# Kernel optimization log

Hardware: AMD Instinct MI355X
Metric: run time of the kernel (lower is better)

Reference implementation:

```python
import jax, jax.numpy as jnp
import numpy as np

B, S, A, M, H, OUT = 256, 256, 256, 256, 8, 256
KD = A // H   # key_dim per head = 32
VD = M // H   # value_dim per head = 32


def setup_inputs() -> dict:
    key = jax.random.key(0)
    ks = jax.random.split(key, 11)
    return {
        "q_data": jax.random.normal(ks[0], (B, S, A), dtype=jnp.float32),
        "m_data": jax.random.normal(ks[1], (B, S, M), dtype=jnp.float32),
        "bias": jax.random.normal(ks[2], (B, 1, 1, S), dtype=jnp.float32),
        "nonbatched_bias": jax.random.normal(ks[3], (H, S, S), dtype=jnp.float32),
        "query_w": jax.random.normal(ks[4], (A, H, KD), dtype=jnp.float32) * 0.05,
        "key_w": jax.random.normal(ks[5], (M, H, KD), dtype=jnp.float32) * 0.05,
        "value_w": jax.random.normal(ks[6], (M, H, VD), dtype=jnp.float32) * 0.05,
        "gating_w": jax.random.normal(ks[7], (A, H, VD), dtype=jnp.float32) * 0.05,
        "gating_b": jax.random.normal(ks[8], (H, VD), dtype=jnp.float32) * 0.05,
        "output_w": jax.random.normal(ks[9], (H, VD, OUT), dtype=jnp.float32) * 0.05,
        "output_b": jax.random.normal(ks[10], (OUT,), dtype=jnp.float32) * 0.05,
    }


def reference(q_data, m_data, bias, nonbatched_bias,
              query_w, key_w, value_w, gating_w, gating_b, output_w, output_b):
    key_dim = query_w.shape[-1]
    # projections
    q = jnp.einsum('bqa,ahc->bqhc', q_data, query_w) * key_dim ** (-0.5)
    k = jnp.einsum('bka,ahc->bkhc', m_data, key_w)
    v = jnp.einsum('bka,ahc->bkhc', m_data, value_w)
    # logits [b,h,q,k] with batched + shared bias
    logits = jnp.einsum('bqhc,bkhc->bhqk', q, k) + bias + nonbatched_bias[None]
    weights = jax.nn.softmax(logits, axis=-1)
    weighted_avg = jnp.einsum('bhqk,bkhc->bqhc', weights, v)
    # sigmoid gating
    gate_values = jax.nn.sigmoid(jnp.einsum('bqc,chv->bqhv', q_data, gating_w) + gating_b)
    weighted_avg = weighted_avg * gate_values
    # output projection
    output = jnp.einsum('bqhc,hco->bqo', weighted_avg, output_w) + output_b
    return output
```

## Files before the change

### kernel.cpp

```cpp
#include <hip/hip_runtime.h>

typedef unsigned short u16;
typedef __attribute__((ext_vector_type(8))) short short8;
typedef __attribute__((ext_vector_type(4))) float f32x4;
typedef __attribute__((ext_vector_type(4))) unsigned int u32x4;
typedef __attribute__((ext_vector_type(4))) unsigned short u16x4;

#define LOG2E 1.4426950408889634f

__device__ __forceinline__ float bf2f(u16 u) {
    union { float f; unsigned int i; } c; c.i = ((unsigned int)u) << 16; return c.f;
}
__device__ __forceinline__ u16 f2bf(float f) {
    unsigned int x = __float_as_uint(f);
    x += 0x7fff + ((x >> 16) & 1);
    return (u16)(x >> 16);
}
__device__ __forceinline__ unsigned int cvtpk(float lo, float hi) {
    unsigned int d;
    asm("v_cvt_pk_bf16_f32 %0, %1, %2" : "=v"(d) : "v"(lo), "v"(hi));
    return d;
}

union Cvt32 { u32x4 v[4]; u16 u[32]; };

__device__ __forceinline__ void ld32f_bf(const float* __restrict__ p, Cvt32& t) {
    union { unsigned int i[8]; u32x4 v[2]; } a;
#pragma unroll
    for (int j = 0; j < 4; j++) {
        f32x4 x = *(const f32x4*)(p + j * 4);
        a.i[j * 2]     = cvtpk(x[0], x[1]);
        a.i[j * 2 + 1] = cvtpk(x[2], x[3]);
    }
    t.v[0] = a.v[0]; t.v[1] = a.v[1];
#pragma unroll
    for (int j = 0; j < 4; j++) {
        f32x4 x = *(const f32x4*)(p + 16 + j * 4);
        a.i[j * 2]     = cvtpk(x[0], x[1]);
        a.i[j * 2 + 1] = cvtpk(x[2], x[3]);
    }
    t.v[2] = a.v[0]; t.v[3] = a.v[1];
}


__global__ __launch_bounds__(256) void prep_a(
    const float* __restrict__ nb,
    const float* __restrict__ qw, const float* __restrict__ kw,
    const float* __restrict__ vw, const float* __restrict__ gw,
    const float* __restrict__ ow,
    u16* __restrict__ wt, u16* __restrict__ WoT, u16* __restrict__ nbT)
{
    __shared__ float tile[64][65];
    int blk = blockIdx.x, tid = threadIdx.x;
    if (blk < 1024) {
        int i = blk * 256 + tid;
        int half = i >> 17;
        int rem = i & 131071;
        int h = rem >> 14, e = rem & 16383;
        int n = e >> 8, k = e & 255;
        int src_idx = k * 256 + h * 32 + (n & 31);
        float v;
        if (half == 0) v = (n < 32) ? kw[src_idx] : vw[src_idx];
        else           v = (n < 32) ? qw[src_idx] : gw[src_idx];
        wt[i] = f2bf(v);
    } else if (blk < 1280) {
        int e = (blk - 1024) * 256 + tid;
        int o = e & 255, hc = e >> 8;
        WoT[o * 256 + hc] = f2bf(ow[hc * 256 + o]);
    } else {
        int idx = blk - 1280;
        int q0 = (idx & 3) * 64, k0 = ((idx >> 2) & 3) * 64, h = idx >> 4;
        int rr = tid >> 4;
        int cc = (tid & 15) << 2;
        const float* src = nb + ((size_t)(h * 256 + q0)) * 256 + k0;
#pragma unroll
        for (int p = 0; p < 4; p++) {
            int q = rr + p * 16;
            f32x4 x = *(const f32x4*)(src + (size_t)q * 256 + cc);
            tile[q][cc] = x[0]; tile[q][cc + 1] = x[1];
            tile[q][cc + 2] = x[2]; tile[q][cc + 3] = x[3];
        }
        __syncthreads();
        u16* dst = nbT + ((size_t)(h * 256 + k0)) * 256 + q0;
#pragma unroll
        for (int p = 0; p < 4; p++) {
            int k = rr + p * 16;
            u16x4 o;
#pragma unroll
            for (int u = 0; u < 4; u++) o[u] = f2bf(tile[cc + u][k] * LOG2E);
            *(u16x4*)(dst + (size_t)k * 256 + cc) = o;
        }
    }
}

__global__ __launch_bounds__(256) void fusedA(
    const float* __restrict__ q_data, const float* __restrict__ m_data,
    const float* __restrict__ bias2, const u16* __restrict__ nbT,
    const u16* __restrict__ wt, const float* __restrict__ gb,
    u16* __restrict__ WA)
{
    __shared__ u16 smem[31488];
    u16* Ksh = smem;
    u16* Vt  = smem + 10240;
    u16* Xs  = smem + 18688;
    u16* Wsh = smem + 28928;

    int bid = blockIdx.x;
    int b = bid >> 3, h = bid & 7;
    int tid = threadIdx.x, lane = tid & 63, w = tid >> 6;
    int l15 = lane & 15;
    int kl = (lane >> 4) << 3;
    int rq = (lane >> 4) << 2;
    const f32x4 fz = {0.f, 0.f, 0.f, 0.f};

    float bload[16];
#pragma unroll
    for (int t = 0; t < 16; t++)
        bload[t] = bias2[(b << 8) + t * 16 + l15] * LOG2E;
    float gbc0 = gb[h * 32 + l15];
    float gbc1 = gb[h * 32 + 16 + l15];

    const float* Xg = m_data + ((size_t)b << 16);
    const u16* Wg = wt + (h << 14);
    f32x4 acc[4][4];
#pragma unroll
    for (int i = 0; i < 4; i++)
#pragma unroll
        for (int j = 0; j < 4; j++) acc[i][j] = fz;

    for (int kb = 0; kb < 8; ++kb) {
        Cvt32 am;
        ld32f_bf(Xg + (size_t)tid * 256 + kb * 32, am);
        u32x4 b0, b1;
        int nrow = tid >> 1, nc = (tid & 1) << 4;
        if (tid < 128) {
            const u16* q = Wg + nrow * 256 + kb * 32 + nc;
            b0 = *(const u32x4*)q; b1 = *(const u32x4*)(q + 8);
        }
        if (kb) __syncthreads();
        *(u32x4*)&Xs[tid * 40]      = am.v[0];
        *(u32x4*)&Xs[tid * 40 + 8]  = am.v[1];
        *(u32x4*)&Xs[tid * 40 + 16] = am.v[2];
        *(u32x4*)&Xs[tid * 40 + 24] = am.v[3];
        if (tid < 128) {
            *(u32x4*)&Wsh[nrow * 40 + nc] = b0;
            *(u32x4*)&Wsh[nrow * 40 + nc + 8] = b1;
        }
        __syncthreads();
        short8 af[4], bf[4];
#pragma unroll
        for (int i = 0; i < 4; i++) af[i] = *(const short8*)&Xs[(64 * w + i * 16 + l15) * 40 + kl];
#pragma unroll
        for (int i = 0; i < 4; i++) bf[i] = *(const short8*)&Wsh[(i * 16 + l15) * 40 + kl];
#pragma unroll
        for (int mi = 0; mi < 4; mi++)
#pragma unroll
            for (int ni = 0; ni < 4; ni++)
                acc[mi][ni] = __builtin_amdgcn_mfma_f32_16x16x32_bf16(af[mi], bf[ni], acc[mi][ni], 0, 0, 0);
    }
#pragma unroll
    for (int mi = 0; mi < 4; mi++)
#pragma unroll
        for (int ni = 0; ni < 4; ni++)
#pragma unroll
            for (int r = 0; r < 4; r++) {
                int s = 64 * w + mi * 16 + rq + r;
                int col = ni * 16 + l15;
                u16 v = f2bf(acc[mi][ni][r]);
                if (ni < 2) Ksh[s * 40 + col] = v;
                else        Vt[(col - 32) * 264 + s] = v;
            }
    __syncthreads();

    const float* Xg2 = q_data + ((size_t)b << 16);
    const u16* Wg2 = wt + 131072 + (h << 14);
    f32x4 acc2[4][4];
#pragma unroll
    for (int i = 0; i < 4; i++)
#pragma unroll
        for (int j = 0; j < 4; j++) acc2[i][j] = fz;

    for (int kb = 0; kb < 8; ++kb) {
        Cvt32 am;
        ld32f_bf(Xg2 + (size_t)tid * 256 + kb * 32, am);
        u32x4 b0, b1;
        int nrow = tid >> 1, nc = (tid & 1) << 4;
        if (tid < 128) {
            const u16* q = Wg2 + nrow * 256 + kb * 32 + nc;
            b0 = *(const u32x4*)q; b1 = *(const u32x4*)(q + 8);
        }
        __syncthreads();
        *(u32x4*)&Xs[tid * 40]      = am.v[0];
        *(u32x4*)&Xs[tid * 40 + 8]  = am.v[1];
        *(u32x4*)&Xs[tid * 40 + 16] = am.v[2];
        *(u32x4*)&Xs[tid * 40 + 24] = am.v[3];
        if (tid < 128) {
            *(u32x4*)&Wsh[nrow * 40 + nc] = b0;
            *(u32x4*)&Wsh[nrow * 40 + nc + 8] = b1;
        }
        __syncthreads();
        short8 af[4], bf[4];
#pragma unroll
        for (int i = 0; i < 4; i++) af[i] = *(const short8*)&Xs[(64 * w + i * 16 + l15) * 40 + kl];
#pragma unroll
        for (int i = 0; i < 4; i++) bf[i] = *(const short8*)&Wsh[(i * 16 + l15) * 40 + kl];
#pragma unroll
        for (int mi = 0; mi < 4; mi++)
#pragma unroll
            for (int ni = 0; ni < 4; ni++)
                acc2[mi][ni] = __builtin_amdgcn_mfma_f32_16x16x32_bf16(af[mi], bf[ni], acc2[mi][ni], 0, 0, 0);
    }
    __syncthreads();

    u16* myQ = smem + 18688 + w * 1792;
    u16* myP = myQ + 640;
    const u16* nbh = nbT + ((size_t)h << 16);
    const float qs = 0.17677669529663687f * LOG2E;
    int orow = lane >> 2, ocol = (lane & 3) << 3;

#pragma unroll
    for (int mt = 0; mt < 4; ++mt) {
        int q0 = 64 * w + mt * 16 + rq;
#pragma unroll
        for (int ni = 0; ni < 2; ++ni)
#pragma unroll
            for (int r = 0; r < 4; r++)
                myQ[(rq + r) * 40 + ni * 16 + l15] = f2bf(acc2[mt][ni][r] * qs);
        short8 qf = *(const short8*)&myQ[l15 * 40 + kl];

        const u16* nbp = nbh + q0;
        float srow[4] = {0.f, 0.f, 0.f, 0.f};
        f32x4 oacc[2] = {fz, fz};
#pragma unroll
        for (int qt = 0; qt < 4; ++qt) {
            f32x4 sc[4];
#pragma unroll
            for (int t = 0; t < 4; t++) {
                int tt = qt * 4 + t;
                short8 kfr = *(const short8*)&Ksh[(tt * 16 + l15) * 40 + kl];
                f32x4 cb = {bload[tt], bload[tt], bload[tt], bload[tt]};
                sc[t] = __builtin_amdgcn_mfma_f32_16x16x32_bf16(qf, kfr, cb, 0, 0, 0);
            }
#pragma unroll
            for (int t = 0; t < 4; t++) {
                int tt = qt * 4 + t;
                u16x4 nbv = *(const u16x4*)(nbp + ((tt * 16 + l15) << 8));
#pragma unroll
                for (int r = 0; r < 4; r++) {
                    float p = __builtin_amdgcn_exp2f(sc[t][r] + bf2f(nbv[r]));
                    srow[r] += p;
                    myP[(rq + r) * 72 + t * 16 + l15] = f2bf(p);
                }
            }
#pragma unroll
            for (int ks = 0; ks < 2; ++ks) {
                short8 pf = *(const short8*)&myP[l15 * 72 + ks * 32 + kl];
#pragma unroll
                for (int ni = 0; ni < 2; ++ni) {
                    short8 vf = *(const short8*)&Vt[(ni * 16 + l15) * 264 + qt * 64 + ks * 32 + kl];
                    oacc[ni] = __builtin_amdgcn_mfma_f32_16x16x32_bf16(pf, vf, oacc[ni], 0, 0, 0);
                }
            }
        }
#pragma unroll
        for (int r = 0; r < 4; r++) {
            float s = srow[r];
            s += __shfl_xor(s, 1);
            s += __shfl_xor(s, 2);
            s += __shfl_xor(s, 4);
            s += __shfl_xor(s, 8);
            srow[r] = __builtin_amdgcn_rcpf(s);
        }

#pragma unroll
        for (int ni = 0; ni < 2; ++ni) {
            float gbv = ni ? gbc1 : gbc0;
#pragma unroll
            for (int r = 0; r < 4; r++) {
                float gate = __builtin_amdgcn_rcpf(
                    1.f + __builtin_amdgcn_exp2f(-(acc2[mt][ni + 2][r] + gbv) * LOG2E));
                myP[(rq + r) * 40 + ni * 16 + l15] = f2bf(oacc[ni][r] * srow[r] * gate);
            }
        }
        u32x4 ov = *(const u32x4*)&myP[orow * 40 + ocol];
        *(u32x4*)(WA + ((size_t)((b << 8) + 64 * w + mt * 16 + orow) << 8) + h * 32 + ocol) = ov;
    }
}

__global__ __launch_bounds__(256) void gemmout_a(
    const u16* __restrict__ WA, const u16* __restrict__ WoT,
    float* __restrict__ dst, const float* __restrict__ ob)
{
    __shared__ u16 As[128 * 40];
    __shared__ u16 Bs[128 * 40];
    int tid = threadIdx.x;
    int lane = tid & 63, w = tid >> 6;
    int wm = w >> 1, wn = w & 1;
    int row0 = blockIdx.x * 128;
    int n0 = blockIdx.y * 128;
    int lr = tid >> 1;
    int lc = (tid & 1) << 4;

    const f32x4 fz = {0.f, 0.f, 0.f, 0.f};
    f32x4 acc[4][4];
#pragma unroll
    for (int i = 0; i < 4; i++)
#pragma unroll
        for (int j = 0; j < 4; j++) acc[i][j] = fz;

    int kl = (lane >> 4) << 3;
    int l15 = lane & 15;
    int rm = wm * 64 + l15;
    int rn = wn * 64 + l15;

    for (int kb = 0; kb < 8; ++kb) {
        int k0 = kb << 5;
        const u16* pa = WA + ((size_t)(row0 + lr) << 8) + k0 + lc;
        u32x4 a0 = *(const u32x4*)pa;
        u32x4 a1 = *(const u32x4*)(pa + 8);
        const u16* pb = WoT + ((size_t)(n0 + lr) << 8) + k0 + lc;
        u32x4 b0 = *(const u32x4*)pb;
        u32x4 b1 = *(const u32x4*)(pb + 8);
        if (kb) __syncthreads();
        *(u32x4*)&As[lr * 40 + lc] = a0;
        *(u32x4*)&As[lr * 40 + lc + 8] = a1;
        *(u32x4*)&Bs[lr * 40 + lc] = b0;
        *(u32x4*)&Bs[lr * 40 + lc + 8] = b1;
        __syncthreads();
        short8 af[4], bf[4];
#pragma unroll
        for (int i = 0; i < 4; i++) af[i] = *(const short8*)&As[(rm + i * 16) * 40 + kl];
#pragma unroll
        for (int i = 0; i < 4; i++) bf[i] = *(const short8*)&Bs[(rn + i * 16) * 40 + kl];
#pragma unroll
        for (int mi = 0; mi < 4; mi++)
#pragma unroll
            for (int ni = 0; ni < 4; ni++)
                acc[mi][ni] = __builtin_amdgcn_mfma_f32_16x16x32_bf16(af[mi], bf[ni], acc[mi][ni], 0, 0, 0);
    }

#pragma unroll
    for (int mi = 0; mi < 4; mi++)
#pragma unroll
        for (int ni = 0; ni < 4; ni++)
#pragma unroll
            for (int r = 0; r < 4; r++) {
                int row = row0 + wm * 64 + mi * 16 + ((lane >> 4) << 2) + r;
                int col = n0 + wn * 64 + ni * 16 + l15;
                dst[((size_t)row << 8) + col] = acc[mi][ni][r] + ob[col];
            }
}


__global__ __launch_bounds__(256) void transpose_k(
    const float* __restrict__ query_w, const float* __restrict__ key_w,
    const float* __restrict__ value_w, const float* __restrict__ gating_w,
    u16* __restrict__ wt)
{
    int i = blockIdx.x * 256 + threadIdx.x;
    int half = i >> 17;
    int rem = i & 131071;
    int h = rem >> 14, e = rem & 16383;
    int n = e >> 8, k = e & 255;
    int src_idx = k * 256 + h * 32 + (n & 31);
    float v;
    if (half == 0) v = (n < 32) ? key_w[src_idx]   : value_w[src_idx];
    else           v = (n < 32) ? query_w[src_idx] : gating_w[src_idx];
    wt[i] = f2bf(v);
}

__global__ __launch_bounds__(256) void fused_attn_k(
    const float* __restrict__ q_data, const float* __restrict__ m_data,
    const float* __restrict__ bias2, const float* __restrict__ nb,
    const u16* __restrict__ wt, const float* __restrict__ gb,
    u16* __restrict__ WAo)
{
    __shared__ u16 smem[31488];
    u16* Ksh = smem;
    u16* Vt  = smem + 10240;
    u16* Xs  = smem + 18688;
    u16* Wsh = smem + 28928;

    int bid = blockIdx.x;
    int b = bid >> 3, h = bid & 7;
    int tid = threadIdx.x, lane = tid & 63, w = tid >> 6;
    int l15 = lane & 15;
    int kl = (lane >> 4) << 3;
    int rq = (lane >> 4) << 2;
    const f32x4 fz = {0.f, 0.f, 0.f, 0.f};

    float bload[16];
#pragma unroll
    for (int t = 0; t < 16; t++) bload[t] = bias2[(b << 8) + t * 16 + l15];
    float gbc0 = gb[h * 32 + l15];
    float gbc1 = gb[h * 32 + 16 + l15];

    const float* Xg = m_data + ((size_t)b << 16);
    const u16* Wg = wt + (h << 14);
    f32x4 acc[4][4];
#pragma unroll
    for (int i = 0; i < 4; i++)
#pragma unroll
        for (int j = 0; j < 4; j++) acc[i][j] = fz;

    for (int kb = 0; kb < 8; ++kb) {
        Cvt32 am;
        ld32f_bf(Xg + (size_t)tid * 256 + kb * 32, am);
        u32x4 b0, b1;
        int nrow = tid >> 1, nc = (tid & 1) << 4;
        if (tid < 128) {
            const u16* q = Wg + nrow * 256 + kb * 32 + nc;
            b0 = *(const u32x4*)q; b1 = *(const u32x4*)(q + 8);
        }
        if (kb) __syncthreads();
        *(u32x4*)&Xs[tid * 40]      = am.v[0];
        *(u32x4*)&Xs[tid * 40 + 8]  = am.v[1];
        *(u32x4*)&Xs[tid * 40 + 16] = am.v[2];
        *(u32x4*)&Xs[tid * 40 + 24] = am.v[3];
        if (tid < 128) {
            *(u32x4*)&Wsh[nrow * 40 + nc] = b0;
            *(u32x4*)&Wsh[nrow * 40 + nc + 8] = b1;
        }
        __syncthreads();
        short8 af[4], bf[4];
#pragma unroll
        for (int i = 0; i < 4; i++) af[i] = *(const short8*)&Xs[(64 * w + i * 16 + l15) * 40 + kl];
#pragma unroll
        for (int i = 0; i < 4; i++) bf[i] = *(const short8*)&Wsh[(i * 16 + l15) * 40 + kl];
#pragma unroll
        for (int mi = 0; mi < 4; mi++)
#pragma unroll
            for (int ni = 0; ni < 4; ni++)
                acc[mi][ni] = __builtin_amdgcn_mfma_f32_16x16x32_bf16(af[mi], bf[ni], acc[mi][ni], 0, 0, 0);
    }
#pragma unroll
    for (int mi = 0; mi < 4; mi++)
#pragma unroll
        for (int ni = 0; ni < 4; ni++)
#pragma unroll
            for (int r = 0; r < 4; r++) {
                int s = 64 * w + mi * 16 + rq + r;
                int col = ni * 16 + l15;
                u16 v = f2bf(acc[mi][ni][r]);
                if (ni < 2) Ksh[s * 40 + col] = v;
                else        Vt[(col - 32) * 264 + s] = v;
            }
    __syncthreads();

    const float* Xg2 = q_data + ((size_t)b << 16);
    const u16* Wg2 = wt + 131072 + (h << 14);
    f32x4 acc2[4][4];
#pragma unroll
    for (int i = 0; i < 4; i++)
#pragma unroll
        for (int j = 0; j < 4; j++) acc2[i][j] = fz;

    for (int kb = 0; kb < 8; ++kb) {
        Cvt32 am;
        ld32f_bf(Xg2 + (size_t)tid * 256 + kb * 32, am);
        u32x4 b0, b1;
        int nrow = tid >> 1, nc = (tid & 1) << 4;
        if (tid < 128) {
            const u16* q = Wg2 + nrow * 256 + kb * 32 + nc;
            b0 = *(const u32x4*)q; b1 = *(const u32x4*)(q + 8);
        }
        __syncthreads();
        *(u32x4*)&Xs[tid * 40]      = am.v[0];
        *(u32x4*)&Xs[tid * 40 + 8]  = am.v[1];
        *(u32x4*)&Xs[tid * 40 + 16] = am.v[2];
        *(u32x4*)&Xs[tid * 40 + 24] = am.v[3];
        if (tid < 128) {
            *(u32x4*)&Wsh[nrow * 40 + nc] = b0;
            *(u32x4*)&Wsh[nrow * 40 + nc + 8] = b1;
        }
        __syncthreads();
        short8 af[4], bf[4];
#pragma unroll
        for (int i = 0; i < 4; i++) af[i] = *(const short8*)&Xs[(64 * w + i * 16 + l15) * 40 + kl];
#pragma unroll
        for (int i = 0; i < 4; i++) bf[i] = *(const short8*)&Wsh[(i * 16 + l15) * 40 + kl];
#pragma unroll
        for (int mi = 0; mi < 4; mi++)
#pragma unroll
            for (int ni = 0; ni < 4; ni++)
                acc2[mi][ni] = __builtin_amdgcn_mfma_f32_16x16x32_bf16(af[mi], bf[ni], acc2[mi][ni], 0, 0, 0);
    }
    __syncthreads();

    u16* myQ = smem + 18688 + w * 2816;
    u16* myP = myQ + 640;
    const float* nbp = nb + ((size_t)h << 16);
    const float qscale = 0.17677669529663687f;

#pragma unroll
    for (int mt = 0; mt < 4; ++mt) {
#pragma unroll
        for (int ni = 0; ni < 2; ++ni)
#pragma unroll
            for (int r = 0; r < 4; r++)
                myQ[(rq + r) * 40 + ni * 16 + l15] = f2bf(acc2[mt][ni][r] * qscale);

        short8 qf = *(const short8*)&myQ[l15 * 40 + kl];
        f32x4 sc[16];
#pragma unroll
        for (int t = 0; t < 16; t++) {
            short8 kfr = *(const short8*)&Ksh[(t * 16 + l15) * 40 + kl];
            sc[t] = __builtin_amdgcn_mfma_f32_16x16x32_bf16(qf, kfr, fz, 0, 0, 0);
        }

        int q0 = 64 * w + mt * 16 + rq;
        float mrow[4] = {-3e30f, -3e30f, -3e30f, -3e30f};
#pragma unroll
        for (int t = 0; t < 16; t++) {
            int kidx = t * 16 + l15;
#pragma unroll
            for (int r = 0; r < 4; r++) {
                float v = sc[t][r] + bload[t] + nbp[(size_t)(q0 + r) * 256 + kidx];
                sc[t][r] = v;
                mrow[r] = fmaxf(mrow[r], v);
            }
        }
#pragma unroll
        for (int r = 0; r < 4; r++) {
            float m = mrow[r];
            m = fmaxf(m, __shfl_xor(m, 1));
            m = fmaxf(m, __shfl_xor(m, 2));
            m = fmaxf(m, __shfl_xor(m, 4));
            m = fmaxf(m, __shfl_xor(m, 8));
            mrow[r] = m;
        }
        float srow[4] = {0.f, 0.f, 0.f, 0.f};
#pragma unroll
        for (int t = 0; t < 16; t++)
#pragma unroll
            for (int r = 0; r < 4; r++) {
                float p = __expf(sc[t][r] - mrow[r]);
                sc[t][r] = p;
                srow[r] += p;
            }
#pragma unroll
        for (int r = 0; r < 4; r++) {
            float s = srow[r];
            s += __shfl_xor(s, 1);
            s += __shfl_xor(s, 2);
            s += __shfl_xor(s, 4);
            s += __shfl_xor(s, 8);
            srow[r] = 1.f / s;
        }

        f32x4 oacc[2] = {fz, fz};
#pragma unroll
        for (int half = 0; half < 2; ++half) {
#pragma unroll
            for (int t = 0; t < 8; t++)
#pragma unroll
                for (int r = 0; r < 4; r++)
                    myP[(rq + r) * 136 + t * 16 + l15] =
                        f2bf(sc[half * 8 + t][r] * srow[r]);
#pragma unroll
            for (int ks = 0; ks < 4; ++ks) {
                short8 pf = *(const short8*)&myP[l15 * 136 + ks * 32 + kl];
#pragma unroll
                for (int ni = 0; ni < 2; ++ni) {
                    short8 vf = *(const short8*)&Vt[(ni * 16 + l15) * 264 + half * 128 + ks * 32 + kl];
                    oacc[ni] = __builtin_amdgcn_mfma_f32_16x16x32_bf16(pf, vf, oacc[ni], 0, 0, 0);
                }
            }
        }

#pragma unroll
        for (int ni = 0; ni < 2; ++ni) {
            float gbv = ni ? gbc1 : gbc0;
#pragma unroll
            for (int r = 0; r < 4; r++) {
                float gate = 1.f / (1.f + __expf(-(acc2[mt][ni + 2][r] + gbv)));
                size_t idx = (((size_t)b << 8) + q0 + r) * 256 + h * 32 + ni * 16 + l15;
                WAo[idx] = f2bf(oacc[ni][r] * gate);
            }
        }
    }
}

__global__ __launch_bounds__(256) void gemm_out_k(
    const u16* __restrict__ X, const float* __restrict__ Wo,
    float* __restrict__ dst, const float* __restrict__ cbias)
{
    __shared__ u16 As[128 * 40];
    __shared__ u16 Bs[128 * 40];
    int tid = threadIdx.x;
    int lane = tid & 63, w = tid >> 6;
    int wm = w >> 1, wn = w & 1;
    int row0 = blockIdx.x * 128;
    int n0 = blockIdx.y * 128;
    int lr = tid >> 1;
    int lc = (tid & 1) << 4;

    const f32x4 fz = {0.f, 0.f, 0.f, 0.f};
    f32x4 acc[4][4];
#pragma unroll
    for (int i = 0; i < 4; i++)
#pragma unroll
        for (int j = 0; j < 4; j++) acc[i][j] = fz;

    int kl = (lane >> 4) << 3;
    int l15 = lane & 15;
    int rm = wm * 64 + l15;
    int rn = wn * 64 + l15;

    for (int kb = 0; kb < 8; ++kb) {
        int k0 = kb << 5;
        const u16* pa = X + ((size_t)(row0 + lr) << 8) + k0 + lc;
        u32x4 a0 = *(const u32x4*)pa;
        u32x4 a1 = *(const u32x4*)(pa + 8);
        int bk = tid >> 3, bn = (tid & 7) << 4;
        const float* pb = Wo + (size_t)(k0 + bk) * 256 + n0 + bn;
        u16 bu[16];
#pragma unroll
        for (int j = 0; j < 16; j += 4) {
            f32x4 x = *(const f32x4*)(pb + j);
            bu[j] = f2bf(x[0]); bu[j + 1] = f2bf(x[1]);
            bu[j + 2] = f2bf(x[2]); bu[j + 3] = f2bf(x[3]);
        }
        if (kb) __syncthreads();
        *(u32x4*)&As[lr * 40 + lc] = a0;
        *(u32x4*)&As[lr * 40 + lc + 8] = a1;
#pragma unroll
        for (int j = 0; j < 16; j++) Bs[(bn + j) * 40 + bk] = bu[j];
        __syncthreads();
        short8 af[4], bf[4];
#pragma unroll
        for (int i = 0; i < 4; i++) af[i] = *(const short8*)&As[(rm + i * 16) * 40 + kl];
#pragma unroll
        for (int i = 0; i < 4; i++) bf[i] = *(const short8*)&Bs[(rn + i * 16) * 40 + kl];
#pragma unroll
        for (int mi = 0; mi < 4; mi++)
#pragma unroll
            for (int ni = 0; ni < 4; ni++)
                acc[mi][ni] = __builtin_amdgcn_mfma_f32_16x16x32_bf16(af[mi], bf[ni], acc[mi][ni], 0, 0, 0);
    }

#pragma unroll
    for (int mi = 0; mi < 4; mi++)
#pragma unroll
        for (int ni = 0; ni < 4; ni++)
#pragma unroll
            for (int r = 0; r < 4; r++) {
                int row = row0 + wm * 64 + mi * 16 + ((lane >> 4) << 2) + r;
                int col = n0 + wn * 64 + ni * 16 + l15;
                dst[((size_t)row << 8) + col] = acc[mi][ni][r] + cbias[col];
            }
}

extern "C" void kernel_launch(void* const* d_in, const int* in_sizes, int n_in,
                              void* d_out, int out_size, void* d_ws, size_t ws_size,
                              hipStream_t stream)
{
    const float* q_data   = (const float*)d_in[0];
    const float* m_data   = (const float*)d_in[1];
    const float* bias     = (const float*)d_in[2];
    const float* nb       = (const float*)d_in[3];
    const float* query_w  = (const float*)d_in[4];
    const float* key_w    = (const float*)d_in[5];
    const float* value_w  = (const float*)d_in[6];
    const float* gating_w = (const float*)d_in[7];
    const float* gating_b = (const float*)d_in[8];
    const float* output_w = (const float*)d_in[9];
    const float* output_b = (const float*)d_in[10];

    const size_t NEED_A = 4ull * 33554432 + 524288 + 131072 + 1048576;

    if (ws_size >= NEED_A) {
        u16* ws   = (u16*)d_ws;
        u16* WA   = ws;
        u16* wt   = WA + 16777216;
        u16* WoT  = wt + 262144;
        u16* nbT  = WoT + 65536;

        prep_a<<<1408, 256, 0, stream>>>(nb, query_w, key_w, value_w, gating_w,
                                         output_w, wt, WoT, nbT);
        fusedA<<<2048, 256, 0, stream>>>(q_data, m_data, bias, nbT, wt, gating_b, WA);
        gemmout_a<<<dim3(512, 2), 256, 0, stream>>>(WA, WoT, (float*)d_out, output_b);
    } else {
        u16* WAb = (u16*)d_ws;
        u16* wt  = (u16*)d_out;
        transpose_k<<<1024, 256, 0, stream>>>(query_w, key_w, value_w, gating_w, wt);
        fused_attn_k<<<2048, 256, 0, stream>>>(q_data, m_data, bias, nb, wt, gating_b, WAb);
        gemm_out_k<<<dim3(512, 2), 256, 0, stream>>>(WAb, output_w, (float*)d_out, output_b);
    }
}
```

Measured before the change: 413.8 us.

## Reorder fusedA projections to alias K into staging LDS and raise occupancy

```diff
diff --git a/kernel.cpp b/kernel.cpp
--- a/kernel.cpp
+++ b/kernel.cpp
@@ -93,17 +93,17 @@
     }
 }
 
-__global__ __launch_bounds__(256) void fusedA(
+__global__ __launch_bounds__(256, 3) void fusedA(
     const float* __restrict__ q_data, const float* __restrict__ m_data,
     const float* __restrict__ bias2, const u16* __restrict__ nbT,
     const u16* __restrict__ wt, const float* __restrict__ gb,
     u16* __restrict__ WA)
 {
-    __shared__ u16 smem[31488];
-    u16* Ksh = smem;
-    u16* Vt  = smem + 10240;
-    u16* Xs  = smem + 18688;
-    u16* Wsh = smem + 28928;
+    __shared__ u16 smem[25856];
+    u16* Vt  = smem;
+    u16* Xs  = smem + 8448;
+    u16* Ksh = Xs;
+    u16* Wsh = smem + 18688;
 
     int bid = blockIdx.x;
     int b = bid >> 3, h = bid & 7;
@@ -120,6 +120,63 @@
     float gbc0 = gb[h * 32 + l15];
     float gbc1 = gb[h * 32 + 16 + l15];
 
+    int srow = tid >> 1;
+    int sc16 = (tid & 1) << 4;
+    int nrow = tid >> 1, nc = (tid & 1) << 4;
+
+    const float* Xg2 = q_data + ((size_t)b << 16);
+    const u16* Wg2 = wt + 131072 + (h << 14);
+    f32x4 acc2[4][4];
+#pragma unroll
+    for (int i = 0; i < 4; i++)
+#pragma unroll
+        for (int j = 0; j < 4; j++) acc2[i][j] = fz;
+
+    for (int kb = 0; kb < 8; ++kb) {
+        u32x4 c0[2], c1[2];
+#pragma unroll
+        for (int p = 0; p < 2; ++p) {
+            const float* ps = Xg2 + (size_t)(p * 128 + srow) * 256 + kb * 32 + sc16;
+            f32x4 x0 = *(const f32x4*)ps;
+            f32x4 x1 = *(const f32x4*)(ps + 4);
+            f32x4 x2 = *(const f32x4*)(ps + 8);
+            f32x4 x3 = *(const f32x4*)(ps + 12);
+            union { unsigned int i4[4]; u32x4 v; } a, c;
+            a.i4[0] = cvtpk(x0[0], x0[1]); a.i4[1] = cvtpk(x0[2], x0[3]);
+            a.i4[2] = cvtpk(x1[0], x1[1]); a.i4[3] = cvtpk(x1[2], x1[3]);
+            c.i4[0] = cvtpk(x2[0], x2[1]); c.i4[1] = cvtpk(x2[2], x2[3]);
+            c.i4[2] = cvtpk(x3[0], x3[1]); c.i4[3] = cvtpk(x3[2], x3[3]);
+            c0[p] = a.v; c1[p] = c.v;
+        }
+        u32x4 b0, b1;
+        if (tid < 128) {
+            const u16* q = Wg2 + nrow * 256 + kb * 32 + nc;
+            b0 = *(const u32x4*)q; b1 = *(const u32x4*)(q + 8);
+        }
+        if (kb) __syncthreads();
+#pragma unroll
+        for (int p = 0; p < 2; ++p) {
+            int row = p * 128 + srow;
+            *(u32x4*)&Xs[row * 40 + sc16]     = c0[p];
+            *(u32x4*)&Xs[row * 40 + sc16 + 8] = c1[p];
+        }
+        if (tid < 128) {
+            *(u32x4*)&Wsh[nrow * 40 + nc] = b0;
+            *(u32x4*)&Wsh[nrow * 40 + nc + 8] = b1;
+        }
+        __syncthreads();
+        short8 af[4], bf[4];
+#pragma unroll
+        for (int i = 0; i < 4; i++) af[i] = *(const short8*)&Xs[(64 * w + i * 16 + l15) * 40 + kl];
+#pragma unroll
+        for (int i = 0; i < 4; i++) bf[i] = *(const short8*)&Wsh[(i * 16 + l15) * 40 + kl];
+#pragma unroll
+        for (int mi = 0; mi < 4; mi++)
+#pragma unroll
+            for (int ni = 0; ni < 4; ni++)
+                acc2[mi][ni] = __builtin_amdgcn_mfma_f32_16x16x32_bf16(af[mi], bf[ni], acc2[mi][ni], 0, 0, 0);
+    }
+
     const float* Xg = m_data + ((size_t)b << 16);
     const u16* Wg = wt + (h << 14);
     f32x4 acc[4][4];
@@ -129,19 +186,33 @@
         for (int j = 0; j < 4; j++) acc[i][j] = fz;
 
     for (int kb = 0; kb < 8; ++kb) {
-        Cvt32 am;
-        ld32f_bf(Xg + (size_t)tid * 256 + kb * 32, am);
+        u32x4 c0[2], c1[2];
+#pragma unroll
+        for (int p = 0; p < 2; ++p) {
+            const float* ps = Xg + (size_t)(p * 128 + srow) * 256 + kb * 32 + sc16;
+            f32x4 x0 = *(const f32x4*)ps;
+            f32x4 x1 = *(const f32x4*)(ps + 4);
+            f32x4 x2 = *(const f32x4*)(ps + 8);
+            f32x4 x3 = *(const f32x4*)(ps + 12);
+            union { unsigned int i4[4]; u32x4 v; } a, c;
+            a.i4[0] = cvtpk(x0[0], x0[1]); a.i4[1] = cvtpk(x0[2], x0[3]);
+            a.i4[2] = cvtpk(x1[0], x1[1]); a.i4[3] = cvtpk(x1[2], x1[3]);
+            c.i4[0] = cvtpk(x2[0], x2[1]); c.i4[1] = cvtpk(x2[2], x2[3]);
+            c.i4[2] = cvtpk(x3[0], x3[1]); c.i4[3] = cvtpk(x3[2], x3[3]);
+            c0[p] = a.v; c1[p] = c.v;
+        }
         u32x4 b0, b1;
-        int nrow = tid >> 1, nc = (tid & 1) << 4;
         if (tid < 128) {
             const u16* q = Wg + nrow * 256 + kb * 32 + nc;
             b0 = *(const u32x4*)q; b1 = *(const u32x4*)(q + 8);
         }
-        if (kb) __syncthreads();
-        *(u32x4*)&Xs[tid * 40]      = am.v[0];
-        *(u32x4*)&Xs[tid * 40 + 8]  = am.v[1];
-        *(u32x4*)&Xs[tid * 40 + 16] = am.v[2];
-        *(u32x4*)&Xs[tid * 40 + 24] = am.v[3];
+        __syncthreads();
+#pragma unroll
+        for (int p = 0; p < 2; ++p) {
+            int row = p * 128 + srow;
+            *(u32x4*)&Xs[row * 40 + sc16]     = c0[p];
+            *(u32x4*)&Xs[row * 40 + sc16 + 8] = c1[p];
+        }
         if (tid < 128) {
             *(u32x4*)&Wsh[nrow * 40 + nc] = b0;
             *(u32x4*)&Wsh[nrow * 40 + nc + 8] = b1;
@@ -172,46 +243,6 @@
             }
     __syncthreads();
 
-    const float* Xg2 = q_data + ((size_t)b << 16);
-    const u16* Wg2 = wt + 131072 + (h << 14);
-    f32x4 acc2[4][4];
-#pragma unroll
-    for (int i = 0; i < 4; i++)
-#pragma unroll
-        for (int j = 0; j < 4; j++) acc2[i][j] = fz;
-
-    for (int kb = 0; kb < 8; ++kb) {
-        Cvt32 am;
-        ld32f_bf(Xg2 + (size_t)tid * 256 + kb * 32, am);
-        u32x4 b0, b1;
-        int nrow = tid >> 1, nc = (tid & 1) << 4;
-        if (tid < 128) {
-            const u16* q = Wg2 + nrow * 256 + kb * 32 + nc;
-            b0 = *(const u32x4*)q; b1 = *(const u32x4*)(q + 8);
-        }
-        __syncthreads();
-        *(u32x4*)&Xs[tid * 40]      = am.v[0];
-        *(u32x4*)&Xs[tid * 40 + 8]  = am.v[1];
-        *(u32x4*)&Xs[tid * 40 + 16] = am.v[2];
-        *(u32x4*)&Xs[tid * 40 + 24] = am.v[3];
-        if (tid < 128) {
-            *(u32x4*)&Wsh[nrow * 40 + nc] = b0;
-            *(u32x4*)&Wsh[nrow * 40 + nc + 8] = b1;
-        }
-        __syncthreads();
-        short8 af[4], bf[4];
-#pragma unroll
-        for (int i = 0; i < 4; i++) af[i] = *(const short8*)&Xs[(64 * w + i * 16 + l15) * 40 + kl];
-#pragma unroll
-        for (int i = 0; i < 4; i++) bf[i] = *(const short8*)&Wsh[(i * 16 + l15) * 40 + kl];
-#pragma unroll
-        for (int mi = 0; mi < 4; mi++)
-#pragma unroll
-            for (int ni = 0; ni < 4; ni++)
-                acc2[mi][ni] = __builtin_amdgcn_mfma_f32_16x16x32_bf16(af[mi], bf[ni], acc2[mi][ni], 0, 0, 0);
-    }
-    __syncthreads();
-
     u16* myQ = smem + 18688 + w * 1792;
     u16* myP = myQ + 640;
     const u16* nbh = nbT + ((size_t)h << 16);
@@ -229,7 +260,7 @@
         short8 qf = *(const short8*)&myQ[l15 * 40 + kl];
 
         const u16* nbp = nbh + q0;
-        float srow[4] = {0.f, 0.f, 0.f, 0.f};
+        float srow_[4] = {0.f, 0.f, 0.f, 0.f};
         f32x4 oacc[2] = {fz, fz};
 #pragma unroll
         for (int qt = 0; qt < 4; ++qt) {
@@ -248,7 +279,7 @@
 #pragma unroll
                 for (int r = 0; r < 4; r++) {
                     float p = __builtin_amdgcn_exp2f(sc[t][r] + bf2f(nbv[r]));
-                    srow[r] += p;
+                    srow_[r] += p;
                     myP[(rq + r) * 72 + t * 16 + l15] = f2bf(p);
                 }
             }
@@ -264,12 +295,12 @@
         }
 #pragma unroll
         for (int r = 0; r < 4; r++) {
-            float s = srow[r];
+            float s = srow_[r];
             s += __shfl_xor(s, 1);
             s += __shfl_xor(s, 2);
             s += __shfl_xor(s, 4);
             s += __shfl_xor(s, 8);
-            srow[r] = __builtin_amdgcn_rcpf(s);
+            srow_[r] = __builtin_amdgcn_rcpf(s);
         }
 
 #pragma unroll
@@ -279,7 +310,7 @@
             for (int r = 0; r < 4; r++) {
                 float gate = __builtin_amdgcn_rcpf(
                     1.f + __builtin_amdgcn_exp2f(-(acc2[mt][ni + 2][r] + gbv) * LOG2E));
-                myP[(rq + r) * 40 + ni * 16 + l15] = f2bf(oacc[ni][r] * srow[r] * gate);
+                myP[(rq + r) * 40 + ni * 16 + l15] = f2bf(oacc[ni][r] * srow_[r] * gate);
             }
         }
         u32x4 ov = *(const u32x4*)&myP[orow * 40 + ocol];
```

Result: slower. 451.5 us (+9.1%).
